# Kernel optimization log

Hardware: AMD Instinct MI355X
Metric: run time of the kernel (lower is better)

The kernel has to match this reference:

```python
import jax, jax.numpy as jnp
import numpy as np

N_FILTERS = 100
WINDOWS = (2, 3, 4, 5)
B, S, W, D = 64, 400, 16, 64
VOCAB, HID = 96, 128


def setup_inputs() -> dict:
    key = jax.random.key(0)
    ks = jax.random.split(key, 16)
    inp = {
        'char_idxs': jax.random.randint(ks[0], (B, S, W), 0, VOCAB),
        'char_vectors': jax.random.normal(ks[1], (VOCAB, D), jnp.float32),
        'filt2': jax.random.normal(ks[2], (N_FILTERS, 2 * D), jnp.float32) * 0.05,
        'filt3': jax.random.normal(ks[3], (N_FILTERS, 3 * D), jnp.float32) * 0.05,
        'filt4': jax.random.normal(ks[4], (N_FILTERS, 4 * D), jnp.float32) * 0.05,
        'filt5': jax.random.normal(ks[5], (N_FILTERS, 5 * D), jnp.float32) * 0.05,
        'w_proj': jax.random.normal(ks[6], (HID, 4 * N_FILTERS), jnp.float32) * 0.05,
        't_w0': jax.random.normal(ks[7], (HID, HID), jnp.float32) * 0.05,
        't_b0': jax.random.normal(ks[8], (HID,), jnp.float32) * 0.05,
        't_w1': jax.random.normal(ks[9], (HID, HID), jnp.float32) * 0.05,
        't_b1': jax.random.normal(ks[10], (HID,), jnp.float32) * 0.05,
        'g_w0': jax.random.normal(ks[11], (HID, HID), jnp.float32) * 0.05,
        'g_b0': jax.random.normal(ks[12], (HID,), jnp.float32) * 0.05,
        'g_w1': jax.random.normal(ks[13], (HID, HID), jnp.float32) * 0.05,
        'g_b1': jax.random.normal(ks[14], (HID,), jnp.float32) * 0.05,
    }
    return inp


def _conv_branch(embed, filt, w):
    # embed: [B, S, W, D]; filt: [100, w*D]
    b, s, wl, d = embed.shape
    L = wl - w + 1  # valid positions
    idx = jnp.arange(L)[:, None] + jnp.arange(w)  # [L, w]
    xw = embed[:, :, idx, :].reshape(b, s, L, w * d)  # [B,S,L,w*D]
    h = jnp.tanh(jnp.einsum('bslk,fk->bslf', xw, filt))  # [B,S,L,100]
    return h.max(axis=2)  # max-pool over all positions -> [B,S,100]


def reference(char_idxs, char_vectors, filt2, filt3, filt4, filt5, w_proj,
              t_w0, t_b0, t_w1, t_b1, g_w0, g_b0, g_w1, g_b1):
    embed = char_vectors[char_idxs]  # [B,S,W,D]
    outs = jnp.concatenate(
        [_conv_branch(embed, f, w) for f, w in zip((filt2, filt3, filt4, filt5), WINDOWS)],
        axis=-1)  # [B,S,400]
    x = outs @ w_proj.T  # no-bias linear -> [B,S,HID]
    # 2-layer highway: x = g*relu(Wt x + bt) + (1-g)*x, g = sigmoid(Wg x + bg)
    for tw, tb, gw, gb in ((t_w0, t_b0, g_w0, g_b0), (t_w1, t_b1, g_w1, g_b1)):
        g = jax.nn.sigmoid(x @ gw.T + gb)
        t = jax.nn.relu(x @ tw.T + tb)
        x = g * t + (1.0 - g) * x
    return x
```

## Files before the change

kernel.cpp:

```cpp
#include <hip/hip_runtime.h>

#define NT     25600
#define WCH    16
#define DIM    64
#define VOCAB  96
#define HID    128
#define KP     416
#define TOKB   64

typedef __attribute__((ext_vector_type(8))) _Float16 h8;
typedef __attribute__((ext_vector_type(4))) float f32x4;
typedef __attribute__((ext_vector_type(4))) int i32x4;

__device__ __forceinline__ float tanh_fast(float m) {
  float t = fminf(fmaxf(m, -9.f), 9.f);
  float e = __builtin_amdgcn_exp2f(t * 2.885390082f);
  return 1.f - 2.f * __builtin_amdgcn_rcpf(e + 1.f);
}

__global__ __launch_bounds__(256) void k_prep(
    const float* __restrict__ cv,
    const float* __restrict__ f2, const float* __restrict__ f3,
    const float* __restrict__ f4, const float* __restrict__ f5,
    const float* __restrict__ wproj,
    const float* __restrict__ tw0, const float* __restrict__ gw0,
    const float* __restrict__ tw1, const float* __restrict__ gw1,
    _Float16* __restrict__ T2, _Float16* __restrict__ wprojP,
    _Float16* __restrict__ hw) {
  __shared__ float fS[100 * 65];
  __shared__ float cvS[8 * 65];
  const int tid = threadIdx.x;
  const int b = blockIdx.x;

  if (b < 168) {
    const int slot = b / 12, cg = b - slot * 12;
    int wi, j;
    if (slot < 2)      { wi = 0; j = slot; }
    else if (slot < 5) { wi = 1; j = slot - 2; }
    else if (slot < 9) { wi = 2; j = slot - 5; }
    else               { wi = 3; j = slot - 9; }
    const float* filt = (wi == 0) ? f2 : (wi == 1) ? f3 : (wi == 2) ? f4 : f5;
    const int rowlen = (wi + 2) * DIM;
    for (int idx = tid; idx < 100 * DIM; idx += 256) {
      int f = idx >> 6, d = idx & 63;
      fS[f * 65 + d] = filt[f * rowlen + j * DIM + d];
    }
    for (int idx = tid; idx < 8 * DIM; idx += 256) {
      int c = idx >> 6, d = idx & 63;
      cvS[c * 65 + d] = cv[(cg * 8 + c) * DIM + d];
    }
    __syncthreads();
    for (int idx = tid; idx < 8 * 104; idx += 256) {
      int cl = idx / 104, f = idx - cl * 104;
      float s = 0.f;
      if (f < 100) {
#pragma unroll 8
        for (int d = 0; d < DIM; ++d) s += cvS[cl * 65 + d] * fS[f * 65 + d];
      }
      T2[((size_t)(f >> 3) * 14 + slot) * 768 + (cg * 8 + cl) * 8 + (f & 7)] =
          (_Float16)s;
    }
  } else if (b < 232) {
    const int n = (b - 168) * 2 + (tid >> 7);
    for (int k = tid & 127; k < KP; k += 128) {
      int s8 = k >> 3;
      int wi = s8 / 13;
      int fl = (s8 - wi * 13) * 8 + (k & 7);
      wprojP[n * KP + k] =
          (fl < 100) ? (_Float16)wproj[n * 400 + wi * 100 + fl] : (_Float16)0.f;
    }
  } else {
    const int idx = (b - 232) * 256 + tid;
    const int which = idx >> 14, r = idx & 16383;
    const float* src = (which == 0) ? tw0 : (which == 1) ? gw0
                     : (which == 2) ? tw1 : gw1;
    hw[idx] = (_Float16)src[r];
  }
}

template<int WI>
__device__ __forceinline__ void conv_g(const _Float16* __restrict__ T2,
                                       const int* __restrict__ ch,
                                       _Float16* __restrict__ convA,
                                       int lane, int o) {
  constexpr int W = WI + 2, L = 15 - WI;
  constexpr int SB = (WI == 0) ? 0 : (WI == 1) ? 2 : (WI == 2) ? 5 : 9;
  const _Float16* Tb = T2 + ((size_t)o * 14 + SB) * 768;
  h8 m;
  {
    h8 s = *(const h8*)(Tb + ch[0]);
#pragma unroll
    for (int j = 1; j < W; ++j) s += *(const h8*)(Tb + j * 768 + ch[j]);
    m = s;
  }
#pragma unroll
  for (int l = 1; l < L; ++l) {
    h8 s = *(const h8*)(Tb + ch[l]);
#pragma unroll
    for (int j = 1; j < W; ++j) s += *(const h8*)(Tb + j * 768 + ch[l + j]);
    m = __builtin_elementwise_max(m, s);
  }
  h8 r;
#pragma unroll
  for (int i = 0; i < 8; ++i) r[i] = (_Float16)tanh_fast((float)m[i]);
  const int s8 = WI * 13 + o;
  *(h8*)(convA + (s8 * 64 + lane) * 8) = r;
}

__global__ __launch_bounds__(512) void k_fused(
    const int* __restrict__ chars,
    const _Float16* __restrict__ T2,
    const _Float16* __restrict__ wprojP,
    const _Float16* __restrict__ hw,
    const float* __restrict__ tb0, const float* __restrict__ tb1,
    const float* __restrict__ gb0, const float* __restrict__ gb1,
    float* __restrict__ out) {
  __shared__ __align__(16) char lds[53248];
  _Float16* convA = (_Float16*)lds;
  _Float16* xA    = (_Float16*)lds;

  const int tid = threadIdx.x;
  const int wave = tid >> 6, lane = tid & 63;
  const int m16 = lane & 15, quad = lane >> 4;
  const int tok0 = blockIdx.x * TOKB;
  const f32x4 zero = {0.f, 0.f, 0.f, 0.f};

  int ch[WCH];
  {
    const i32x4* cp = (const i32x4*)(chars + (size_t)(tok0 + lane) * WCH);
#pragma unroll
    for (int q = 0; q < 4; ++q) {
      i32x4 v = cp[q];
#pragma unroll
      for (int i = 0; i < 4; ++i) ch[q * 4 + i] = v[i] * 8;
    }
  }

  switch (wave) {
    case 0: for (int o = 0;  o < 5;  ++o) conv_g<3>(T2, ch, convA, lane, o); break;
    case 1: for (int o = 5;  o < 10; ++o) conv_g<3>(T2, ch, convA, lane, o); break;
    case 2: for (int o = 10; o < 13; ++o) conv_g<3>(T2, ch, convA, lane, o);
            for (int o = 0;  o < 2;  ++o) conv_g<2>(T2, ch, convA, lane, o); break;
    case 3: for (int o = 2;  o < 8;  ++o) conv_g<2>(T2, ch, convA, lane, o); break;
    case 4: for (int o = 8;  o < 13; ++o) conv_g<2>(T2, ch, convA, lane, o);
            conv_g<0>(T2, ch, convA, lane, 0); break;
    case 5: for (int o = 0;  o < 7;  ++o) conv_g<1>(T2, ch, convA, lane, o); break;
    case 6: for (int o = 7;  o < 13; ++o) conv_g<1>(T2, ch, convA, lane, o);
            conv_g<0>(T2, ch, convA, lane, 1); break;
    default: for (int o = 2; o < 13; ++o) conv_g<0>(T2, ch, convA, lane, o); break;
  }
  __syncthreads();

  const int hc = wave * 16 + m16;
  f32x4 xp[4];
#pragma unroll
  for (int mt = 0; mt < 4; ++mt) xp[mt] = zero;

  for (int ks = 0; ks < 13; ++ks) {
    const int s8 = ks * 4 + quad;
    h8 b = *(const h8*)(wprojP + (size_t)hc * KP + s8 * 8);
#pragma unroll
    for (int mt = 0; mt < 4; ++mt) {
      h8 a = *(const h8*)(convA + (s8 * 64 + mt * 16 + m16) * 8);
      xp[mt] = __builtin_amdgcn_mfma_f32_16x16x32_f16(a, b, xp[mt], 0, 0, 0);
    }
  }
  __syncthreads();

#pragma unroll
  for (int mt = 0; mt < 4; ++mt)
#pragma unroll
    for (int r = 0; r < 4; ++r)
      xA[(hc >> 3) * 512 + (mt * 16 + quad * 4 + r) * 8 + (hc & 7)] =
          (_Float16)xp[mt][r];
  __syncthreads();

#pragma unroll
  for (int layer = 0; layer < 2; ++layer) {
    const _Float16* tw = hw + (layer ? 2 : 0) * HID * HID;
    const _Float16* gw = hw + (layer ? 3 : 1) * HID * HID;
    const float* tbv = layer ? tb1 : tb0;
    const float* gbv = layer ? gb1 : gb0;
    float bt = tbv[hc], bg = gbv[hc];

    f32x4 at[4], ag[4];
#pragma unroll
    for (int mt = 0; mt < 4; ++mt) { at[mt] = zero; ag[mt] = zero; }

#pragma unroll
    for (int ks = 0; ks < 4; ++ks) {
      const int ko = ks * 32 + quad * 8;
      h8 btw = *(const h8*)(tw + (size_t)hc * HID + ko);
      h8 bgw = *(const h8*)(gw + (size_t)hc * HID + ko);
#pragma unroll
      for (int mt = 0; mt < 4; ++mt) {
        h8 a = *(const h8*)(xA + (ks * 4 + quad) * 512 + (mt * 16 + m16) * 8);
        at[mt] = __builtin_amdgcn_mfma_f32_16x16x32_f16(a, btw, at[mt], 0, 0, 0);
        ag[mt] = __builtin_amdgcn_mfma_f32_16x16x32_f16(a, bgw, ag[mt], 0, 0, 0);
      }
    }
    __syncthreads();

#pragma unroll
    for (int mt = 0; mt < 4; ++mt)
#pragma unroll
      for (int r = 0; r < 4; ++r) {
        float g = 1.f / (1.f + __builtin_amdgcn_exp2f(
                             -(ag[mt][r] + bg) * 1.442695041f));
        float tt = fmaxf(at[mt][r] + bt, 0.f);
        float xn = g * tt + (1.f - g) * xp[mt][r];
        xp[mt][r] = xn;
        int row = mt * 16 + quad * 4 + r;
        if (layer == 0)
          xA[(hc >> 3) * 512 + row * 8 + (hc & 7)] = (_Float16)xn;
        else
          out[(size_t)(tok0 + row) * HID + hc] = xn;
      }
    if (layer == 0) __syncthreads();
  }
}

extern "C" void kernel_launch(void* const* d_in, const int* in_sizes, int n_in,
                              void* d_out, int out_size, void* d_ws, size_t ws_size,
                              hipStream_t stream) {
  (void)in_sizes; (void)n_in; (void)out_size; (void)ws_size;
  const int* chars = (const int*)d_in[0];
  const float* cv  = (const float*)d_in[1];
  const float* f2  = (const float*)d_in[2];
  const float* f3  = (const float*)d_in[3];
  const float* f4  = (const float*)d_in[4];
  const float* f5  = (const float*)d_in[5];
  const float* wpj = (const float*)d_in[6];
  const float* tw0 = (const float*)d_in[7];
  const float* tb0 = (const float*)d_in[8];
  const float* tw1 = (const float*)d_in[9];
  const float* tb1 = (const float*)d_in[10];
  const float* gw0 = (const float*)d_in[11];
  const float* gb0 = (const float*)d_in[12];
  const float* gw1 = (const float*)d_in[13];
  const float* gb1 = (const float*)d_in[14];
  float* out = (float*)d_out;

  char* ws = (char*)d_ws;
  _Float16* T2     = (_Float16*)ws;
  _Float16* wprojP = (_Float16*)(ws + 279552);
  _Float16* hw     = (_Float16*)(ws + 279552 + 106496);

  k_prep<<<488, 256, 0, stream>>>(cv, f2, f3, f4, f5, wpj, tw0, gw0, tw1, gw1,
                                  T2, wprojP, hw);
  k_fused<<<NT / TOKB, 512, 0, stream>>>(chars, T2, wprojP, hw,
                                         tb0, tb1, gb0, gb1, out);
}
```

Measured before the change: 180.1 us.

## Split conv into LDS-staged per-window kernel writing global intermediate, then head kernel

Moves the character-convolution gather out of the fused kernel into a separate kernel where each block serves one window size, stages that window's precomputed table slices (up to 5 slots) in LDS, and gathers from LDS instead of global/L2. The conv outputs go to a global fp16 buffer that a second head kernel reads back for the projection and highway MFMAs. The table layout changes to slot-major with a 104 stride. A fallback fused path is kept for small workspaces. It trades L2 gather traffic for an extra ~26MB round trip and one more launch.

```diff
diff --git a/kernel.cpp b/kernel.cpp
--- a/kernel.cpp
+++ b/kernel.cpp
@@ -7,6 +7,7 @@
 #define HID    128
 #define KP     416
 #define TOKB   64
+#define SLOT   9984
 
 typedef __attribute__((ext_vector_type(8))) _Float16 h8;
 typedef __attribute__((ext_vector_type(4))) float f32x4;
@@ -25,7 +26,7 @@
     const float* __restrict__ wproj,
     const float* __restrict__ tw0, const float* __restrict__ gw0,
     const float* __restrict__ tw1, const float* __restrict__ gw1,
-    _Float16* __restrict__ T2, _Float16* __restrict__ wprojP,
+    _Float16* __restrict__ T3, _Float16* __restrict__ wprojP,
     _Float16* __restrict__ hw) {
   __shared__ float fS[100 * 65];
   __shared__ float cvS[8 * 65];
@@ -57,8 +58,7 @@
 #pragma unroll 8
         for (int d = 0; d < DIM; ++d) s += cvS[cl * 65 + d] * fS[f * 65 + d];
       }
-      T2[((size_t)(f >> 3) * 14 + slot) * 768 + (cg * 8 + cl) * 8 + (f & 7)] =
-          (_Float16)s;
+      T3[((size_t)slot * 96 + cg * 8 + cl) * 104 + f] = (_Float16)s;
     }
   } else if (b < 232) {
     const int n = (b - 168) * 2 + (tid >> 7);
@@ -79,37 +79,78 @@
 }
 
 template<int WI>
-__device__ __forceinline__ void conv_g(const _Float16* __restrict__ T2,
-                                       const int* __restrict__ ch,
-                                       _Float16* __restrict__ convA,
-                                       int lane, int o) {
+__device__ __forceinline__ void conv_block(const int* __restrict__ chars,
+                                           const _Float16* __restrict__ Ts,
+                                           _Float16* __restrict__ convG,
+                                           int t0, int TC) {
   constexpr int W = WI + 2, L = 15 - WI;
-  constexpr int SB = (WI == 0) ? 0 : (WI == 1) ? 2 : (WI == 2) ? 5 : 9;
-  const _Float16* Tb = T2 + ((size_t)o * 14 + SB) * 768;
-  h8 m;
-  {
-    h8 s = *(const h8*)(Tb + ch[0]);
-#pragma unroll
-    for (int j = 1; j < W; ++j) s += *(const h8*)(Tb + j * 768 + ch[j]);
-    m = s;
-  }
-#pragma unroll
-  for (int l = 1; l < L; ++l) {
-    h8 s = *(const h8*)(Tb + ch[l]);
-#pragma unroll
-    for (int j = 1; j < W; ++j) s += *(const h8*)(Tb + j * 768 + ch[l + j]);
-    m = __builtin_elementwise_max(m, s);
-  }
-  h8 r;
-#pragma unroll
-  for (int i = 0; i < 8; ++i) r[i] = (_Float16)tanh_fast((float)m[i]);
-  const int s8 = WI * 13 + o;
-  *(h8*)(convA + (s8 * 64 + lane) * 8) = r;
-}
-
-__global__ __launch_bounds__(512) void k_fused(
-    const int* __restrict__ chars,
-    const _Float16* __restrict__ T2,
+  const int nit = TC * 13;
+  for (int it = threadIdx.x; it < nit; it += 512) {
+    const int oct = it / TC, tloc = it - oct * TC;
+    const int token = t0 + tloc;
+    int ch[WCH];
+    {
+      const i32x4* cp = (const i32x4*)(chars + (size_t)token * WCH);
+#pragma unroll
+      for (int q = 0; q < 4; ++q) {
+        i32x4 v = cp[q];
+#pragma unroll
+        for (int i = 0; i < 4; ++i) ch[q * 4 + i] = v[i] * 104;
+      }
+    }
+    const _Float16* Tb = Ts + oct * 8;
+    h8 m;
+    {
+      h8 s = *(const h8*)(Tb + ch[0]);
+#pragma unroll
+      for (int j = 1; j < W; ++j) s += *(const h8*)(Tb + j * SLOT + ch[j]);
+      m = s;
+    }
+#pragma unroll
+    for (int l = 1; l < L; ++l) {
+      h8 s = *(const h8*)(Tb + ch[l]);
+#pragma unroll
+      for (int j = 1; j < W; ++j) s += *(const h8*)(Tb + j * SLOT + ch[l + j]);
+      m = __builtin_elementwise_max(m, s);
+    }
+    h8 r;
+#pragma unroll
+    for (int i = 0; i < 8; ++i) r[i] = (_Float16)tanh_fast((float)m[i]);
+    const int s8 = WI * 13 + oct;
+    *(h8*)(convG + ((size_t)s8 * NT + token) * 8) = r;
+  }
+}
+
+__global__ __launch_bounds__(512) void k_conv(const int* __restrict__ chars,
+                                              const _Float16* __restrict__ T3,
+                                              _Float16* __restrict__ convG) {
+  __shared__ __align__(16) _Float16 Ts[5 * SLOT];
+  const int b = blockIdx.x;
+  int wi, b0, TC;
+  if (b < 100)      { wi = 0; b0 = 0;   TC = 256; }
+  else if (b < 260) { wi = 1; b0 = 100; TC = 160; }
+  else if (b < 420) { wi = 2; b0 = 260; TC = 160; }
+  else              { wi = 3; b0 = 420; TC = 128; }
+  const int W = wi + 2;
+  const int SB = (wi == 0) ? 0 : (wi == 1) ? 2 : (wi == 2) ? 5 : 9;
+  const int t0 = (b - b0) * TC;
+
+  const _Float16* src = T3 + (size_t)SB * SLOT;
+  const int nchunk = W * (SLOT / 8);
+  for (int r = threadIdx.x; r < nchunk; r += 512)
+    *(h8*)(Ts + r * 8) = *(const h8*)(src + r * 8);
+  __syncthreads();
+
+  switch (wi) {
+    case 0: conv_block<0>(chars, Ts, convG, t0, TC); break;
+    case 1: conv_block<1>(chars, Ts, convG, t0, TC); break;
+    case 2: conv_block<2>(chars, Ts, convG, t0, TC); break;
+    default: conv_block<3>(chars, Ts, convG, t0, TC); break;
+  }
+}
+
+__global__ __launch_bounds__(512) void k_head(
+    const _Float16* __restrict__ convG,
     const _Float16* __restrict__ wprojP,
     const _Float16* __restrict__ hw,
     const float* __restrict__ tb0, const float* __restrict__ tb1,
@@ -125,29 +166,9 @@
   const int tok0 = blockIdx.x * TOKB;
   const f32x4 zero = {0.f, 0.f, 0.f, 0.f};
 
-  int ch[WCH];
-  {
-    const i32x4* cp = (const i32x4*)(chars + (size_t)(tok0 + lane) * WCH);
-#pragma unroll
-    for (int q = 0; q < 4; ++q) {
-      i32x4 v = cp[q];
-#pragma unroll
-      for (int i = 0; i < 4; ++i) ch[q * 4 + i] = v[i] * 8;
-    }
-  }
-
-  switch (wave) {
-    case 0: for (int o = 0;  o < 5;  ++o) conv_g<3>(T2, ch, convA, lane, o); break;
-    case 1: for (int o = 5;  o < 10; ++o) conv_g<3>(T2, ch, convA, lane, o); break;
-    case 2: for (int o = 10; o < 13; ++o) conv_g<3>(T2, ch, convA, lane, o);
-            for (int o = 0;  o < 2;  ++o) conv_g<2>(T2, ch, convA, lane, o); break;
-    case 3: for (int o = 2;  o < 8;  ++o) conv_g<2>(T2, ch, convA, lane, o); break;
-    case 4: for (int o = 8;  o < 13; ++o) conv_g<2>(T2, ch, convA, lane, o);
-            conv_g<0>(T2, ch, convA, lane, 0); break;
-    case 5: for (int o = 0;  o < 7;  ++o) conv_g<1>(T2, ch, convA, lane, o); break;
-    case 6: for (int o = 7;  o < 13; ++o) conv_g<1>(T2, ch, convA, lane, o);
-            conv_g<0>(T2, ch, convA, lane, 1); break;
-    default: for (int o = 2; o < 13; ++o) conv_g<0>(T2, ch, convA, lane, o); break;
+  for (int g = wave; g < 52; g += 8) {
+    h8 v = *(const h8*)(convG + ((size_t)g * NT + tok0 + lane) * 8);
+    *(h8*)(convA + (g * 64 + lane) * 8) = v;
   }
   __syncthreads();
 
@@ -220,10 +241,146 @@
   }
 }
 
+template<int WI>
+__device__ __forceinline__ void conv_g(const _Float16* __restrict__ T3,
+                                       const int* __restrict__ ch,
+                                       _Float16* __restrict__ convA,
+                                       int lane, int o) {
+  constexpr int W = WI + 2, L = 15 - WI;
+  constexpr int SB = (WI == 0) ? 0 : (WI == 1) ? 2 : (WI == 2) ? 5 : 9;
+  const _Float16* Tb = T3 + (size_t)SB * SLOT + o * 8;
+  h8 m;
+  {
+    h8 s = *(const h8*)(Tb + ch[0]);
+#pragma unroll
+    for (int j = 1; j < W; ++j) s += *(const h8*)(Tb + j * SLOT + ch[j]);
+    m = s;
+  }
+#pragma unroll
+  for (int l = 1; l < L; ++l) {
+    h8 s = *(const h8*)(Tb + ch[l]);
+#pragma unroll
+    for (int j = 1; j < W; ++j) s += *(const h8*)(Tb + j * SLOT + ch[l + j]);
+    m = __builtin_elementwise_max(m, s);
+  }
+  h8 r;
+#pragma unroll
+  for (int i = 0; i < 8; ++i) r[i] = (_Float16)tanh_fast((float)m[i]);
+  const int s8 = WI * 13 + o;
+  *(h8*)(convA + (s8 * 64 + lane) * 8) = r;
+}
+
+__global__ __launch_bounds__(512) void k_fb(
+    const int* __restrict__ chars,
+    const _Float16* __restrict__ T3,
+    const _Float16* __restrict__ wprojP,
+    const _Float16* __restrict__ hw,
+    const float* __restrict__ tb0, const float* __restrict__ tb1,
+    const float* __restrict__ gb0, const float* __restrict__ gb1,
+    float* __restrict__ out) {
+  __shared__ __align__(16) char lds[53248];
+  _Float16* convA = (_Float16*)lds;
+  _Float16* xA    = (_Float16*)lds;
+
+  const int tid = threadIdx.x;
+  const int wave = tid >> 6, lane = tid & 63;
+  const int m16 = lane & 15, quad = lane >> 4;
+  const int tok0 = blockIdx.x * TOKB;
+  const f32x4 zero = {0.f, 0.f, 0.f, 0.f};
+
+  int ch[WCH];
+  {
+    const i32x4* cp = (const i32x4*)(chars + (size_t)(tok0 + lane) * WCH);
+#pragma unroll
+    for (int q = 0; q < 4; ++q) {
+      i32x4 v = cp[q];
+#pragma unroll
+      for (int i = 0; i < 4; ++i) ch[q * 4 + i] = v[i] * 104;
+    }
+  }
+
+  switch (wave) {
+    case 0: for (int o = 0;  o < 5;  ++o) conv_g<3>(T3, ch, convA, lane, o); break;
+    case 1: for (int o = 5;  o < 10; ++o) conv_g<3>(T3, ch, convA, lane, o); break;
+    case 2: for (int o = 10; o < 13; ++o) conv_g<3>(T3, ch, convA, lane, o);
+            for (int o = 0;  o < 2;  ++o) conv_g<2>(T3, ch, convA, lane, o); break;
+    case 3: for (int o = 2;  o < 8;  ++o) conv_g<2>(T3, ch, convA, lane, o); break;
+    case 4: for (int o = 8;  o < 13; ++o) conv_g<2>(T3, ch, convA, lane, o);
+            conv_g<0>(T3, ch, convA, lane, 0); break;
+    case 5: for (int o = 0;  o < 7;  ++o) conv_g<1>(T3, ch, convA, lane, o); break;
+    case 6: for (int o = 7;  o < 13; ++o) conv_g<1>(T3, ch, convA, lane, o);
+            conv_g<0>(T3, ch, convA, lane, 1); break;
+    default: for (int o = 2; o < 13; ++o) conv_g<0>(T3, ch, convA, lane, o); break;
+  }
+  __syncthreads();
+
+  const int hc = wave * 16 + m16;
+  f32x4 xp[4];
+#pragma unroll
+  for (int mt = 0; mt < 4; ++mt) xp[mt] = zero;
+  for (int ks = 0; ks < 13; ++ks) {
+    const int s8 = ks * 4 + quad;
+    h8 b = *(const h8*)(wprojP + (size_t)hc * KP + s8 * 8);
+#pragma unroll
+    for (int mt = 0; mt < 4; ++mt) {
+      h8 a = *(const h8*)(convA + (s8 * 64 + mt * 16 + m16) * 8);
+      xp[mt] = __builtin_amdgcn_mfma_f32_16x16x32_f16(a, b, xp[mt], 0, 0, 0);
+    }
+  }
+  __syncthreads();
+#pragma unroll
+  for (int mt = 0; mt < 4; ++mt)
+#pragma unroll
+    for (int r = 0; r < 4; ++r)
+      xA[(hc >> 3) * 512 + (mt * 16 + quad * 4 + r) * 8 + (hc & 7)] =
+          (_Float16)xp[mt][r];
+  __syncthreads();
+#pragma unroll
+  for (int layer = 0; layer < 2; ++layer) {
+    const _Float16* tw = hw + (layer ? 2 : 0) * HID * HID;
+    const _Float16* gw = hw + (layer ? 3 : 1) * HID * HID;
+    const float* tbv = layer ? tb1 : tb0;
+    const float* gbv = layer ? gb1 : gb0;
+    float bt = tbv[hc], bg = gbv[hc];
+    f32x4 at[4], ag[4];
+#pragma unroll
+    for (int mt = 0; mt < 4; ++mt) { at[mt] = zero; ag[mt] = zero; }
+#pragma unroll
+    for (int ks = 0; ks < 4; ++ks) {
+      const int ko = ks * 32 + quad * 8;
+      h8 btw = *(const h8*)(tw + (size_t)hc * HID + ko);
+      h8 bgw = *(const h8*)(gw + (size_t)hc * HID + ko);
+#pragma unroll
+      for (int mt = 0; mt < 4; ++mt) {
+        h8 a = *(const h8*)(xA + (ks * 4 + quad) * 512 + (mt * 16 + m16) * 8);
+        at[mt] = __builtin_amdgcn_mfma_f32_16x16x32_f16(a, btw, at[mt], 0, 0, 0);
+        ag[mt] = __builtin_amdgcn_mfma_f32_16x16x32_f16(a, bgw, ag[mt], 0, 0, 0);
+      }
+    }
+    __syncthreads();
+#pragma unroll
+    for (int mt = 0; mt < 4; ++mt)
+#pragma unroll
+      for (int r = 0; r < 4; ++r) {
+        float g = 1.f / (1.f + __builtin_amdgcn_exp2f(
+                             -(ag[mt][r] + bg) * 1.442695041f));
+        float tt = fmaxf(at[mt][r] + bt, 0.f);
+        float xn = g * tt + (1.f - g) * xp[mt][r];
+        xp[mt][r] = xn;
+        int row = mt * 16 + quad * 4 + r;
+        if (layer == 0)
+          xA[(hc >> 3) * 512 + row * 8 + (hc & 7)] = (_Float16)xn;
+        else
+          out[(size_t)(tok0 + row) * HID + hc] = xn;
+      }
+    if (layer == 0) __syncthreads();
+  }
+}
+
 extern "C" void kernel_launch(void* const* d_in, const int* in_sizes, int n_in,
                               void* d_out, int out_size, void* d_ws, size_t ws_size,
                               hipStream_t stream) {
-  (void)in_sizes; (void)n_in; (void)out_size; (void)ws_size;
+  (void)in_sizes; (void)n_in; (void)out_size;
   const int* chars = (const int*)d_in[0];
   const float* cv  = (const float*)d_in[1];
   const float* f2  = (const float*)d_in[2];
@@ -242,12 +399,19 @@
   float* out = (float*)d_out;
 
   char* ws = (char*)d_ws;
-  _Float16* T2     = (_Float16*)ws;
+  _Float16* T3     = (_Float16*)ws;
   _Float16* wprojP = (_Float16*)(ws + 279552);
-  _Float16* hw     = (_Float16*)(ws + 279552 + 106496);
+  _Float16* hw     = (_Float16*)(ws + 386048);
+  _Float16* convG  = (_Float16*)(ws + 517120);
 
   k_prep<<<488, 256, 0, stream>>>(cv, f2, f3, f4, f5, wpj, tw0, gw0, tw1, gw1,
-                                  T2, wprojP, hw);
-  k_fused<<<NT / TOKB, 512, 0, stream>>>(chars, T2, wprojP, hw,
-                                         tb0, tb1, gb0, gb1, out);
-}
+                                  T3, wprojP, hw);
+  if (ws_size >= (size_t)21816320) {
+    k_conv<<<620, 512, 0, stream>>>(chars, T3, convG);
+    k_head<<<NT / TOKB, 512, 0, stream>>>(convG, wprojP, hw,
+                                          tb0, tb1, gb0, gb1, out);
+  } else {
+    k_fb<<<NT / TOKB, 512, 0, stream>>>(chars, T3, wprojP, hw,
+                                        tb0, tb1, gb0, gb1, out);
+  }
+}
```

New measurement: 152.1 us. 1.18x faster.
